# Performance work log

Measured on AMD Instinct MI355X. Metric: run time of the kernel, lower is better.

The kernel has to match this reference:

```python
import jax, jax.numpy as jnp
import numpy as np

B, N, K, D, H, L = 2, 2048, 256, 768, 150, 11
REL_PROP = 2
NB = 10  # distance buckets


def _lin(key, din, dout):
    return jax.random.normal(key, (din, dout), dtype=jnp.float32) / np.sqrt(din)


def setup_inputs() -> dict:
    key = jax.random.key(0)
    ks = jax.random.split(key, 16)
    rng = np.random.default_rng(0)
    prune_idx = jnp.asarray(np.stack([np.sort(rng.permutation(N)[:K]) for _ in range(B)]), dtype=jnp.int32)
    span_begin = jnp.sort(jax.random.randint(ks[2], (B, K), 0, N - 16), axis=-1).astype(jnp.int32)
    span_end = (span_begin + jax.random.randint(ks[3], (B, K), 1, 16)).astype(jnp.int32)
    return {
        "all_span_vecs": jax.random.normal(ks[0], (B, N, D), dtype=jnp.float32),
        "update": jax.random.normal(ks[1], (B, K, D), dtype=jnp.float32),
        "square_mask": jnp.ones((B, K, K), dtype=jnp.float32),
        "span_lengths": jnp.full((B,), float(K), dtype=jnp.float32),
        "span_begin": span_begin,
        "span_end": span_end,
        "prune_indices": prune_idx,
        "w_left": _lin(ks[4], D, H), "b_left": jnp.zeros((H,), jnp.float32),
        "w_right": _lin(ks[5], D, H), "b_right": jnp.zeros((H,), jnp.float32),
        "dist_emb": jax.random.normal(ks[6], (NB, H), dtype=jnp.float32) * 0.02,
        "w_h": _lin(ks[7], H, H), "b_h": jnp.zeros((H,), jnp.float32),
        "w_out": _lin(ks[8], H, L), "b_out": jnp.zeros((L,), jnp.float32),
        "a_w": _lin(ks[9], L, D),
        "gate_w": _lin(ks[10], 2 * D, D), "gate_b": jnp.zeros((D,), jnp.float32),
        "pr_w": _lin(ks[11], D, 1), "pr_b": jnp.zeros((1,), jnp.float32),
    }


def _pair_scores(u, bins, w_left, b_left, w_right, b_right, dist_emb, w_h, b_h, w_out, b_out):
    # OptFFpairs: left/right span projections + pairwise distance embedding -> FF -> L labels
    left = u @ w_left + b_left          # [B,K,H]
    right = u @ w_right + b_right       # [B,K,H]
    h = jax.nn.relu(left[:, :, None, :] + right[:, None, :, :] + dist_emb[bins])  # [B,K,K,H]
    h = jax.nn.relu(h @ w_h + b_h)
    return h @ w_out + b_out            # [B,K,K,L]


def _add_unary(rel, ss):
    # relation_add_scores: add per-span pruner scores along both pair axes; ss: [B,K,1]
    return rel + ss[:, :, None, :] + ss[:, None, :, :]


def reference(all_span_vecs, update, square_mask, span_lengths, span_begin, span_end,
              prune_indices, w_left, b_left, w_right, b_right, dist_emb, w_h, b_h,
              w_out, b_out, a_w, gate_w, gate_b, pr_w, pr_b):
    bins = jnp.clip(jnp.abs(span_begin[:, None, :] - span_begin[:, :, None]), 0, NB - 1)  # [B,K,K]
    rel = _pair_scores(update, bins, w_left, b_left, w_right, b_right, dist_emb, w_h, b_h, w_out, b_out)
    rel = _add_unary(rel, update @ pr_w + pr_b)
    for _ in range(REL_PROP):
        probs = jax.nn.relu(rel) * square_mask[..., None]     # [B,K,K,L]
        msg = probs @ a_w                                     # A(probs): [B,K,K,D]
        # ctxt[b,j,d] = sum_i msg[b,i,j,d] * update[b,i,d] / span_lengths[b]
        ctxt = (msg * update[:, :, None, :]).sum(-3) / span_lengths[:, None, None]
        g = jax.nn.sigmoid(jnp.concatenate([update, ctxt], axis=-1) @ gate_w + gate_b)
        update = g * update + (1.0 - g) * ctxt                # MyGate
        rel = _pair_scores(update, bins, w_left, b_left, w_right, b_right, dist_emb, w_h, b_h, w_out, b_out)
        rel = _add_unary(rel, update @ pr_w + pr_b)           # pruner.scorer(update)
    # overwrite_spans: scatter updated filtered spans back into the full span tensor
    valid = jnp.arange(K)[None, :] < span_lengths[:, None]    # [B,K]
    bidx = jnp.arange(B)[:, None]
    orig = all_span_vecs[bidx, prune_indices]                 # [B,K,D]
    vals = jnp.where(valid[..., None], update, orig)
    update_all = all_span_vecs.at[bidx, prune_indices].set(vals)
    return update_all, update, rel
```

## Files before the change

### kernel.cpp

```cpp
#include <hip/hip_runtime.h>
#include <hip/hip_bf16.h>
#include <math.h>

#define BB 2
#define NN 2048
#define KK 256
#define DD 768
#define HH 150
#define LL 11
#define NBINS 10

#define KP 160
#define WP 40
#define GWP 72
#define BPAD 264

typedef __attribute__((ext_vector_type(8))) short short8;
typedef __attribute__((ext_vector_type(4))) short s16x4;
typedef __attribute__((ext_vector_type(4))) float f32x4;

__device__ inline unsigned bf2u(float lo, float hi) {
  union { __hip_bfloat162 b; unsigned u; } cv;
  cv.b = __float22bfloat162_rn(make_float2(lo, hi));
  return cv.u;
}
__device__ inline short bf1(float x) {
  union { __hip_bfloat16 b; short s; } cv;
  cv.b = __float2bfloat16(x);
  return cv.s;
}

__global__ void k_prep(const float* __restrict__ w_h, const float* __restrict__ w_out,
                       short* __restrict__ wt, short* __restrict__ wo) {
  int idx = blockIdx.x * 256 + threadIdx.x;
  if (idx < KP * KP) {
    int n = idx / KP, k = idx - n * KP;
    float v = (n < HH && k < HH) ? w_h[k * HH + n] : 0.f;
    wt[idx] = bf1(v);
  }
  int idx2 = idx - KP * KP;
  if (idx2 >= 0 && idx2 < 16 * KP) {
    int n = idx2 / KP, k = idx2 - n * KP;
    float v = (n < LL && k < HH) ? w_out[k * LL + n] : 0.f;
    wo[idx2] = bf1(v);
  }
}

__global__ void k_cvt(const float* __restrict__ src, short* __restrict__ dst, int n) {
  int idx = blockIdx.x * 256 + threadIdx.x;
  if (idx < n) dst[idx] = bf1(src[idx]);
}

__global__ __launch_bounds__(256) void k_tr_gw(const float* __restrict__ gate_w,
                                               short* __restrict__ gwt) {
  __shared__ float tile[32][33];
  int kt = blockIdx.x % 48, nt = blockIdx.x / 48;
  int m0 = kt * 32, n0 = nt * 32;
  int tx = threadIdx.x & 31, ty = threadIdx.x >> 5;
  #pragma unroll
  for (int r = 0; r < 4; ++r)
    tile[ty + r * 8][tx] = gate_w[(size_t)(m0 + ty + r * 8) * DD + n0 + tx];
  __syncthreads();
  #pragma unroll
  for (int r = 0; r < 4; ++r)
    gwt[(size_t)(n0 + ty + r * 8) * (2 * DD) + m0 + tx] = bf1(tile[tx][ty + r * 8]);
}

__global__ __launch_bounds__(256) void k_tr_wlr(const float* __restrict__ w_left,
                                                const float* __restrict__ w_right,
                                                short* __restrict__ wlrt) {
  __shared__ float tile[32][33];
  int kt = blockIdx.x % 24, nt = blockIdx.x / 24;
  int k0 = kt * 32, n0 = nt * 32;
  const float* src = (n0 >= KP) ? w_right : w_left;
  int col0 = n0 - (n0 >= KP ? KP : 0);
  int tx = threadIdx.x & 31, ty = threadIdx.x >> 5;
  #pragma unroll
  for (int r = 0; r < 4; ++r) {
    int col = col0 + tx;
    tile[ty + r * 8][tx] = (col < HH) ? src[(size_t)(k0 + ty + r * 8) * HH + col] : 0.f;
  }
  __syncthreads();
  #pragma unroll
  for (int r = 0; r < 4; ++r)
    wlrt[(size_t)(n0 + ty + r * 8) * DD + k0 + tx] = bf1(tile[tx][ty + r * 8]);
}

__global__ __launch_bounds__(256) void k_tr_upd(const float* __restrict__ upd,
                                                short* __restrict__ updT) {
  __shared__ float tile[32][33];
  int bidx = blockIdx.x;
  int b = bidx / 192;
  int r = bidx - b * 192;
  int it = r & 7, dt = r >> 3;
  int i0 = it * 32, d0 = dt * 32;
  int tx = threadIdx.x & 31, ty = threadIdx.x >> 5;
  #pragma unroll
  for (int rr = 0; rr < 4; ++rr)
    tile[ty + rr * 8][tx] = upd[(size_t)(b * KK + i0 + ty + rr * 8) * DD + d0 + tx];
  __syncthreads();
  #pragma unroll
  for (int rr = 0; rr < 4; ++rr)
    updT[(size_t)(b * DD + d0 + ty + rr * 8) * KK + i0 + tx] = bf1(tile[tx][ty + rr * 8]);
}

__global__ __launch_bounds__(256) void k_ptr(const float* __restrict__ rel,
                                             const float* __restrict__ mask,
                                             short* __restrict__ probsT) {
  __shared__ float tile[32][353];
  __shared__ float maskS[32][32];
  int bidx = blockIdx.x;
  int b = bidx >> 6;
  int r = bidx & 63;
  int it = r >> 3, jt = r & 7;
  int i0 = it * 32, j0 = jt * 32;
  int t = threadIdx.x;
  for (int idx = t; idx < 32 * 352; idx += 256) {
    int ii = idx / 352, c = idx - ii * 352;
    tile[ii][c] = rel[(((size_t)(b * KK + i0 + ii)) * KK + j0) * LL + c];
  }
  for (int idx = t; idx < 1024; idx += 256) {
    int ii = idx >> 5, jj = idx & 31;
    maskS[ii][jj] = mask[((size_t)(b * KK + i0 + ii)) * KK + j0 + jj];
  }
  __syncthreads();
  for (int idx = t; idx < LL * 512; idx += 256) {
    int l = idx / 512;
    int rem = idx - l * 512;
    int jj = rem >> 4, ii = (rem & 15) * 2;
    float v0 = fmaxf(tile[ii][jj * LL + l], 0.f) * maskS[ii][jj];
    float v1 = fmaxf(tile[ii + 1][jj * LL + l], 0.f) * maskS[ii + 1][jj];
    *(unsigned*)(probsT + (((size_t)(b * LL + l)) * KK + j0 + jj) * KK + i0 + ii) =
        bf2u(v0, v1);
  }
}

__global__ __launch_bounds__(256) void k_ss(const float* __restrict__ upd,
                                            const float* __restrict__ pr_w,
                                            const float* __restrict__ pr_b,
                                            float* __restrict__ ss) {
  int row = blockIdx.x * 4 + (threadIdx.x >> 6);
  int l = threadIdx.x & 63;
  float s = 0.f;
  for (int d = l; d < DD; d += 64) s = fmaf(upd[(size_t)row * DD + d], pr_w[d], s);
  #pragma unroll
  for (int off = 32; off > 0; off >>= 1) s += __shfl_down(s, off);
  if (l == 0) ss[row] = s + pr_b[0];
}

__global__ __launch_bounds__(256) void k_proj_mfma(
    const short* __restrict__ updbf, const short* __restrict__ wlrt,
    const float* __restrict__ b_left, const float* __restrict__ b_right,
    float* __restrict__ left, float* __restrict__ right)
{
  int rbk = blockIdx.x >> 1, half = blockIdx.x & 1;
  int row0 = rbk * 64;
  const short* wsrc = wlrt + (size_t)half * KP * DD;
  __shared__ short As[64][WP];
  __shared__ short Bs[KP][WP];
  int t = threadIdx.x, l = t & 63, w = t >> 6, lr = l & 15, lg = l >> 4;
  int ar = t >> 2, ac = t & 3;
  int i1 = t + 256, i2 = t + 512;
  f32x4 acc[10];
  #pragma unroll
  for (int nt = 0; nt < 10; ++nt) acc[nt] = (f32x4){0.f, 0.f, 0.f, 0.f};

  short8 pa, pb0, pb1, pb2 = {};
  pa  = *(const short8*)(updbf + (size_t)(row0 + ar) * DD + ac * 8);
  pb0 = *(const short8*)(wsrc + (size_t)(t >> 2) * DD + (t & 3) * 8);
  pb1 = *(const short8*)(wsrc + (size_t)(i1 >> 2) * DD + (i1 & 3) * 8);
  if (i2 < 640) pb2 = *(const short8*)(wsrc + (size_t)(i2 >> 2) * DD + (i2 & 3) * 8);

  for (int ks = 0; ks < 24; ++ks) {
    __syncthreads();
    *(short8*)&As[ar][ac * 8] = pa;
    *(short8*)&Bs[t >> 2][(t & 3) * 8] = pb0;
    *(short8*)&Bs[i1 >> 2][(i1 & 3) * 8] = pb1;
    if (i2 < 640) *(short8*)&Bs[i2 >> 2][(i2 & 3) * 8] = pb2;
    __syncthreads();
    if (ks + 1 < 24) {
      int k0 = (ks + 1) * 32;
      pa  = *(const short8*)(updbf + (size_t)(row0 + ar) * DD + k0 + ac * 8);
      pb0 = *(const short8*)(wsrc + (size_t)(t >> 2) * DD + k0 + (t & 3) * 8);
      pb1 = *(const short8*)(wsrc + (size_t)(i1 >> 2) * DD + k0 + (i1 & 3) * 8);
      if (i2 < 640) pb2 = *(const short8*)(wsrc + (size_t)(i2 >> 2) * DD + k0 + (i2 & 3) * 8);
    }
    short8 a = *(short8*)&As[w * 16 + lr][lg * 8];
    #pragma unroll
    for (int nt = 0; nt < 10; ++nt) {
      short8 b = *(short8*)&Bs[nt * 16 + lr][lg * 8];
      acc[nt] = __builtin_amdgcn_mfma_f32_16x16x32_bf16(a, b, acc[nt], 0, 0, 0);
    }
  }
  const float* bias = half ? b_right : b_left;
  float* dst = half ? right : left;
  int rowb = row0 + w * 16 + lg * 4;
  #pragma unroll
  for (int nt = 0; nt < 10; ++nt) {
    int col = nt * 16 + lr;
    if (col < HH) {
      float bv = bias[col];
      #pragma unroll
      for (int q = 0; q < 4; ++q)
        dst[(size_t)(rowb + q) * HH + col] = acc[nt][q] + bv;
    }
  }
}

__global__ __launch_bounds__(256, 4) void k_pair_mfma(
    const float* __restrict__ left, const float* __restrict__ right,
    const float* __restrict__ ss, const int* __restrict__ span_begin,
    const float* __restrict__ demb,
    const short* __restrict__ wt, const short* __restrict__ wo,
    const float* __restrict__ b_h, const float* __restrict__ b_out,
    float* __restrict__ rel)
{
  int bid = blockIdx.x;
  int b  = bid >> 10;
  int r2 = bid & 1023;
  int i  = r2 >> 2;
  int j0 = (r2 & 3) * 64;

  __shared__ short wtbuf[2][32 * KP];
  __shared__ float ld_s[NBINS][KP];
  __shared__ float bh_s[KP];
  __shared__ float ssj_s[64];
  __shared__ int   bins[64];

  int t = threadIdx.x;
  int l = t & 63, w = t >> 6;
  int lr = l & 15, lg = l >> 4;

  int jr = w * 16 + lr;
  const float* rrow = right + (size_t)(b * KK + j0 + jr) * HH;
  float2 rv[20];
  #pragma unroll
  for (int ks = 0; ks < 5; ++ks) {
    #pragma unroll
    for (int e = 0; e < 4; ++e) {
      int k = ks * 32 + lg * 8 + e * 2;
      rv[ks * 4 + e] = (k < HH - 1) ? *(const float2*)(rrow + k) : make_float2(0.f, 0.f);
    }
  }

  int sbi = span_begin[b * KK + i];
  if (t < 64) {
    int d = span_begin[b * KK + j0 + t] - sbi; d = d < 0 ? -d : d;
    bins[t] = d > NBINS - 1 ? NBINS - 1 : d;
    ssj_s[t] = ss[b * KK + j0 + t];
  }
  for (int idx = t; idx < KP; idx += 256) bh_s[idx] = (idx < HH) ? b_h[idx] : 0.f;
  {
    const float* lrow = left + (size_t)(b * KK + i) * HH;
    for (int idx = t; idx < NBINS * KP; idx += 256) {
      int bn = idx / KP, k = idx - bn * KP;
      ld_s[bn][k] = (k < HH) ? (lrow[k] + demb[bn * HH + k]) : 0.f;
    }
  }
  short8 wo_f[5];
  #pragma unroll
  for (int ks = 0; ks < 5; ++ks)
    wo_f[ks] = *(const short8*)(wo + lr * KP + ks * 32 + lg * 8);

  short8 pw[3];
  #pragma unroll
  for (int c = 0; c < 3; ++c) {
    int idx = t + c * 256;
    if (idx < 640) pw[c] = *(const short8*)(wt + idx * 8);
  }
  #pragma unroll
  for (int c = 0; c < 3; ++c) {
    int idx = t + c * 256;
    if (idx < 640) *(short8*)&wtbuf[0][idx * 8] = pw[c];
  }
  #pragma unroll
  for (int c = 0; c < 3; ++c) {
    int idx = t + c * 256;
    if (idx < 640) pw[c] = *(const short8*)(wt + 5120 + idx * 8);
  }
  __syncthreads();

  int binr = bins[jr];
  const float* ldr = &ld_s[binr][0];
  short8 afr[5];
  #pragma unroll
  for (int ks = 0; ks < 5; ++ks) {
    unsigned pk[4];
    #pragma unroll
    for (int e = 0; e < 4; ++e) {
      int k = ks * 32 + lg * 8 + e * 2;
      float2 lv = *(const float2*)(ldr + k);
      float2 r2v = rv[ks * 4 + e];
      float v0 = fmaxf(lv.x + r2v.x, 0.f);
      float v1 = fmaxf(lv.y + r2v.y, 0.f);
      pk[e] = bf2u(v0, v1);
    }
    int4 tmp; tmp.x = (int)pk[0]; tmp.y = (int)pk[1]; tmp.z = (int)pk[2]; tmp.w = (int)pk[3];
    afr[ks] = *(short8*)&tmp;
  }

  f32x4 acc[10];
  #pragma unroll
  for (int m = 0; m < 10; ++m) acc[m] = (f32x4){0.f, 0.f, 0.f, 0.f};

  #pragma unroll
  for (int s = 0; s < 5; ++s) {
    if (s > 0) __syncthreads();
    if (s + 1 < 5) {
      #pragma unroll
      for (int c = 0; c < 3; ++c) {
        int idx = t + c * 256;
        if (idx < 640) *(short8*)&wtbuf[(s + 1) & 1][idx * 8] = pw[c];
      }
      if (s + 2 < 5) {
        #pragma unroll
        for (int c = 0; c < 3; ++c) {
          int idx = t + c * 256;
          if (idx < 640) pw[c] = *(const short8*)(wt + (s + 2) * 5120 + idx * 8);
        }
      }
    }
    const short* bufp = &wtbuf[s & 1][0];
    #pragma unroll
    for (int ks = 0; ks < 5; ++ks) {
      short8 a = afr[ks];
      #pragma unroll
      for (int ntp = 0; ntp < 2; ++ntp) {
        short8 bf = *(const short8*)(bufp + (ntp * 16 + lr) * KP + ks * 32 + lg * 8);
        acc[s * 2 + ntp] = __builtin_amdgcn_mfma_f32_16x16x32_bf16(a, bf, acc[s * 2 + ntp], 0, 0, 0);
      }
    }
  }
  __syncthreads();

  short* h1 = &wtbuf[0][0];
  #pragma unroll
  for (int m = 0; m < 10; ++m) {
    int col = (m >> 1) * 32 + (m & 1) * 16 + lr;
    float bh = bh_s[col];
    #pragma unroll
    for (int q = 0; q < 4; ++q) {
      int row = w * 16 + lg * 4 + q;
      h1[row * KP + col] = bf1(fmaxf(acc[m][q] + bh, 0.f));
    }
  }
  __syncthreads();

  f32x4 acc2 = (f32x4){0.f, 0.f, 0.f, 0.f};
  #pragma unroll
  for (int ks = 0; ks < 5; ++ks) {
    short8 a = *(const short8*)(h1 + (w * 16 + lr) * KP + ks * 32 + lg * 8);
    acc2 = __builtin_amdgcn_mfma_f32_16x16x32_bf16(a, wo_f[ks], acc2, 0, 0, 0);
  }

  float ssi = ss[b * KK + i];
  float* out_s = (float*)&ld_s[0][0];
  if (lr < LL) {
    float bo = b_out[lr];
    #pragma unroll
    for (int q = 0; q < 4; ++q) {
      int row = w * 16 + lg * 4 + q;
      out_s[row * 12 + lr] = acc2[q] + bo + ssi + ssj_s[row];
    }
  }
  __syncthreads();
  size_t base = ((size_t)(b * KK + i) * KK + j0) * LL;
  for (int idx = t; idx < 64 * LL; idx += 256) {
    int j = idx / LL, ll2 = idx - j * LL;
    rel[base + idx] = out_s[j * 12 + ll2];
  }
}

__global__ __launch_bounds__(256) void k_ctxt_mfma(
    const short* __restrict__ probsT, const short* __restrict__ updT,
    const float* __restrict__ a_w, const float* __restrict__ span_len,
    float* __restrict__ ctxt, short* __restrict__ ctxbf)
{
  int bidx = blockIdx.x;
  int b = bidx / 96;
  int r = bidx - b * 96;
  int jt = r / 12, dt = r - jt * 12;
  int j0 = jt * 32, d0 = dt * 64;

  __shared__ short Bs[64][BPAD];
  __shared__ short As[32][BPAD];

  int t = threadIdx.x, l = t & 63, w = t >> 6, lr = l & 15, lg = l >> 4;
  int wr = w >> 1, wc = w & 1;

  for (int s = 0; s < 8; ++s) {
    int idx = t + s * 256;
    int row = idx >> 5, c = idx & 31;
    *(short8*)&Bs[row][c * 8] =
        *(const short8*)(updT + ((size_t)(b * DD + d0 + row)) * KK + c * 8);
  }

  short8 pa[4];
  #pragma unroll
  for (int s = 0; s < 4; ++s) {
    int idx = t + s * 256;
    int row = idx >> 5, c = idx & 31;
    pa[s] = *(const short8*)(probsT + (((size_t)(b * LL + 0)) * KK + j0 + row) * KK + c * 8);
  }

  f32x4 accF[2];
  accF[0] = (f32x4){0.f, 0.f, 0.f, 0.f};
  accF[1] = (f32x4){0.f, 0.f, 0.f, 0.f};

  for (int ll = 0; ll < LL; ++ll) {
    __syncthreads();
    #pragma unroll
    for (int s = 0; s < 4; ++s) {
      int idx = t + s * 256;
      int row = idx >> 5, c = idx & 31;
      *(short8*)&As[row][c * 8] = pa[s];
    }
    if (ll + 1 < LL) {
      #pragma unroll
      for (int s = 0; s < 4; ++s) {
        int idx = t + s * 256;
        int row = idx >> 5, c = idx & 31;
        pa[s] = *(const short8*)(probsT + (((size_t)(b * LL + ll + 1)) * KK + j0 + row) * KK + c * 8);
      }
    }
    float awl[2];
    #pragma unroll
    for (int nt = 0; nt < 2; ++nt) awl[nt] = a_w[ll * DD + d0 + wc * 32 + nt * 16 + lr];
    __syncthreads();

    f32x4 accL[2];
    accL[0] = (f32x4){0.f, 0.f, 0.f, 0.f};
    accL[1] = (f32x4){0.f, 0.f, 0.f, 0.f};
    #pragma unroll
    for (int ks = 0; ks < 8; ++ks) {
      short8 a = *(short8*)&As[wr * 16 + lr][ks * 32 + lg * 8];
      #pragma unroll
      for (int nt = 0; nt < 2; ++nt) {
        short8 bf = *(short8*)&Bs[wc * 32 + nt * 16 + lr][ks * 32 + lg * 8];
        accL[nt] = __builtin_amdgcn_mfma_f32_16x16x32_bf16(a, bf, accL[nt], 0, 0, 0);
      }
    }
    #pragma unroll
    for (int nt = 0; nt < 2; ++nt)
      #pragma unroll
      for (int q = 0; q < 4; ++q)
        accF[nt][q] = fmaf(awl[nt], accL[nt][q], accF[nt][q]);
  }

  float inv = 1.f / span_len[b];
  int rowb = j0 + wr * 16 + lg * 4;
  #pragma unroll
  for (int nt = 0; nt < 2; ++nt) {
    int col = d0 + wc * 32 + nt * 16 + lr;
    #pragma unroll
    for (int q = 0; q < 4; ++q) {
      size_t off = (size_t)(b * KK + rowb + q) * DD + col;
      float v = accF[nt][q] * inv;
      ctxt[off] = v;
      ctxbf[off] = bf1(v);
    }
  }
}

__global__ __launch_bounds__(256) void k_gate_mfma(
    const short* __restrict__ updbf, const short* __restrict__ ctxbf,
    const short* __restrict__ gwt, const float* __restrict__ gate_b,
    const float* __restrict__ ctxt, float* __restrict__ upd,
    short* __restrict__ nxtbf, short* __restrict__ updT)
{
  int rb = blockIdx.x / 12, cb = blockIdx.x - rb * 12;
  int row0 = rb * 32, col0 = cb * 64;
  __shared__ short As[32][GWP];
  __shared__ short Bs[64][GWP];
  int t = threadIdx.x, l = t & 63, w = t >> 6, lr = l & 15, lg = l >> 4;
  int wr = w >> 1, wc = w & 1;

  int ar = t >> 3, ac = t & 7;
  int b1 = t + 256;

  f32x4 acc[2];
  acc[0] = (f32x4){0.f, 0.f, 0.f, 0.f};
  acc[1] = (f32x4){0.f, 0.f, 0.f, 0.f};

  short8 pa = *(const short8*)(updbf + (size_t)(row0 + ar) * DD + ac * 8);
  short8 pb0 = *(const short8*)(gwt + (size_t)(col0 + (t >> 3)) * (2 * DD) + (t & 7) * 8);
  short8 pb1 = *(const short8*)(gwt + (size_t)(col0 + (b1 >> 3)) * (2 * DD) + (b1 & 7) * 8);

  for (int ks = 0; ks < 24; ++ks) {
    __syncthreads();
    *(short8*)&As[ar][ac * 8] = pa;
    *(short8*)&Bs[t >> 3][(t & 7) * 8] = pb0;
    *(short8*)&Bs[b1 >> 3][(b1 & 7) * 8] = pb1;
    if (ks + 1 < 24) {
      int k0 = (ks + 1) * 64;
      int ka = k0 + ac * 8;
      const short* asrc = (ka < DD) ? (updbf + (size_t)(row0 + ar) * DD + ka)
                                    : (ctxbf + (size_t)(row0 + ar) * DD + ka - DD);
      pa  = *(const short8*)asrc;
      pb0 = *(const short8*)(gwt + (size_t)(col0 + (t >> 3)) * (2 * DD) + k0 + (t & 7) * 8);
      pb1 = *(const short8*)(gwt + (size_t)(col0 + (b1 >> 3)) * (2 * DD) + k0 + (b1 & 7) * 8);
    }
    __syncthreads();
    #pragma unroll
    for (int ksub = 0; ksub < 2; ++ksub) {
      short8 a = *(short8*)&As[wr * 16 + lr][ksub * 32 + lg * 8];
      #pragma unroll
      for (int nt = 0; nt < 2; ++nt) {
        short8 bf = *(short8*)&Bs[wc * 32 + nt * 16 + lr][ksub * 32 + lg * 8];
        acc[nt] = __builtin_amdgcn_mfma_f32_16x16x32_bf16(a, bf, acc[nt], 0, 0, 0);
      }
    }
  }
  int rowb = row0 + wr * 16 + lg * 4;
  int bb = rowb >> 8, ii = rowb & 255;
  #pragma unroll
  for (int nt = 0; nt < 2; ++nt) {
    int col = col0 + wc * 32 + nt * 16 + lr;
    float gb = gate_b[col];
    s16x4 tw;
    #pragma unroll
    for (int q = 0; q < 4; ++q) {
      size_t off = (size_t)(rowb + q) * DD + col;
      float x = acc[nt][q] + gb;
      float g = 1.f / (1.f + expf(-x));
      float o = g * upd[off] + (1.f - g) * ctxt[off];
      upd[off] = o;
      short bv = bf1(o);
      nxtbf[off] = bv;
      tw[q] = bv;
    }
    *(s16x4*)(updT + ((size_t)(bb * DD + col)) * KK + ii) = tw;
  }
}

__global__ void k_scatter(const float* __restrict__ upd,
                          const int* __restrict__ prune_idx,
                          const float* __restrict__ span_len,
                          float* __restrict__ out_all)
{
  int b = blockIdx.x / KK;
  int k = blockIdx.x - b * KK;
  if ((float)k < span_len[b]) {
    int dst = prune_idx[b * KK + k];
    const float4* src = (const float4*)(upd + ((size_t)(b * KK + k)) * DD);
    float4* d = (float4*)(out_all + ((size_t)b * NN + dst) * DD);
    for (int idx = threadIdx.x; idx < DD / 4; idx += blockDim.x) d[idx] = src[idx];
  }
}

extern "C" void kernel_launch(void* const* d_in, const int* in_sizes, int n_in,
                              void* d_out, int out_size, void* d_ws, size_t ws_size,
                              hipStream_t stream)
{
  (void)in_sizes; (void)n_in; (void)out_size; (void)ws_size;
  const float* all_span = (const float*)d_in[0];
  const float* upd_in   = (const float*)d_in[1];
  const float* mask     = (const float*)d_in[2];
  const float* span_len = (const float*)d_in[3];
  const int*   span_beg = (const int*)d_in[4];
  const int*   prune    = (const int*)d_in[6];
  const float* w_left   = (const float*)d_in[7];
  const float* b_left   = (const float*)d_in[8];
  const float* w_right  = (const float*)d_in[9];
  const float* b_right  = (const float*)d_in[10];
  const float* dist_emb = (const float*)d_in[11];
  const float* w_h      = (const float*)d_in[12];
  const float* b_h      = (const float*)d_in[13];
  const float* w_out    = (const float*)d_in[14];
  const float* b_out    = (const float*)d_in[15];
  const float* a_w      = (const float*)d_in[16];
  const float* gate_w   = (const float*)d_in[17];
  const float* gate_b   = (const float*)d_in[18];
  const float* pr_w     = (const float*)d_in[19];
  const float* pr_b     = (const float*)d_in[20];

  float* out_all = (float*)d_out;
  float* out_upd = out_all + (size_t)BB * NN * DD;
  float* out_rel = out_upd + (size_t)BB * KK * DD;

  float* ws     = (float*)d_ws;
  float* left   = ws;
  float* right  = left + (size_t)BB * KK * HH;
  float* ssv    = right + (size_t)BB * KK * HH + 64;
  float* ctxt   = ssv + (size_t)BB * KK;
  short* wt_bf  = (short*)(ctxt + (size_t)BB * KK * DD);
  short* wo_bf  = wt_bf + KP * KP;
  short* updbf0 = wo_bf + 16 * KP;
  short* updbf1 = updbf0 + (size_t)BB * KK * DD;
  short* ctxbf  = updbf1 + (size_t)BB * KK * DD;
  short* gwt    = ctxbf + (size_t)BB * KK * DD;
  short* wlrt   = gwt + (size_t)DD * 2 * DD;
  short* probsT = wlrt + (size_t)2 * KP * DD;
  short* updT   = probsT + (size_t)BB * LL * KK * KK;

  const int nupd = BB * KK * DD;

  hipMemcpyAsync(out_all, all_span, sizeof(float) * (size_t)BB * NN * DD,
                 hipMemcpyDeviceToDevice, stream);
  hipMemcpyAsync(out_upd, upd_in, sizeof(float) * (size_t)BB * KK * DD,
                 hipMemcpyDeviceToDevice, stream);
  k_prep<<<(KP * KP + 16 * KP + 255) / 256, 256, 0, stream>>>(w_h, w_out, wt_bf, wo_bf);
  k_cvt<<<(nupd + 255) / 256, 256, 0, stream>>>(upd_in, updbf0, nupd);
  k_tr_gw<<<48 * 24, 256, 0, stream>>>(gate_w, gwt);
  k_tr_wlr<<<24 * 10, 256, 0, stream>>>(w_left, w_right, wlrt);
  k_tr_upd<<<BB * 8 * 24, 256, 0, stream>>>(upd_in, updT);

  k_proj_mfma<<<16, 256, 0, stream>>>(updbf0, wlrt, b_left, b_right, left, right);
  k_ss<<<BB * KK / 4, 256, 0, stream>>>(out_upd, pr_w, pr_b, ssv);
  k_pair_mfma<<<BB * KK * 4, 256, 0, stream>>>(left, right, ssv, span_beg, dist_emb,
                                               wt_bf, wo_bf, b_h, b_out, out_rel);

  for (int p = 0; p < 2; ++p) {
    short* cur_bf = (p == 0) ? updbf0 : updbf1;
    short* nxt_bf = (p == 0) ? updbf1 : updbf0;
    k_ptr<<<BB * 8 * 8, 256, 0, stream>>>(out_rel, mask, probsT);
    k_ctxt_mfma<<<BB * 8 * 12, 256, 0, stream>>>(probsT, updT, a_w, span_len, ctxt, ctxbf);
    k_gate_mfma<<<16 * 12, 256, 0, stream>>>(cur_bf, ctxbf, gwt, gate_b, ctxt,
                                             out_upd, nxt_bf, updT);
    k_proj_mfma<<<16, 256, 0, stream>>>(nxt_bf, wlrt, b_left, b_right, left, right);
    k_ss<<<BB * KK / 4, 256, 0, stream>>>(out_upd, pr_w, pr_b, ssv);
    k_pair_mfma<<<BB * KK * 4, 256, 0, stream>>>(left, right, ssv, span_beg, dist_emb,
                                                 wt_bf, wo_bf, b_h, b_out, out_rel);
  }
  k_scatter<<<BB * KK, 192, 0, stream>>>(out_upd, prune, span_len, out_all);
}
```

Before: 231.7 us.

## Fuse prep kernels, merge proj with ss, emit probsT from pair kernel

Merges the five preprocessing kernels into one multi-role launch, and folds the unary score reduction into the projection kernel as extra blocks. The pair-score kernel gains a templated epilogue that writes the masked, relu'd, transposed bf16 probabilities directly, removing the separate transpose kernel and its re-read of rel. The right-row operand loads also move from an upfront register array into the inner loop to cut register pressure. The price is strided 2-byte scattered stores for probsT from the pair kernel, and blocks of different roles running inside single launches.

```diff
diff --git a/kernel.cpp b/kernel.cpp
--- a/kernel.cpp
+++ b/kernel.cpp
@@ -30,135 +30,122 @@
   return cv.s;
 }
 
-__global__ void k_prep(const float* __restrict__ w_h, const float* __restrict__ w_out,
-                       short* __restrict__ wt, short* __restrict__ wo) {
-  int idx = blockIdx.x * 256 + threadIdx.x;
-  if (idx < KP * KP) {
-    int n = idx / KP, k = idx - n * KP;
-    float v = (n < HH && k < HH) ? w_h[k * HH + n] : 0.f;
-    wt[idx] = bf1(v);
-  }
-  int idx2 = idx - KP * KP;
-  if (idx2 >= 0 && idx2 < 16 * KP) {
-    int n = idx2 / KP, k = idx2 - n * KP;
-    float v = (n < LL && k < HH) ? w_out[k * LL + n] : 0.f;
-    wo[idx2] = bf1(v);
-  }
-}
-
-__global__ void k_cvt(const float* __restrict__ src, short* __restrict__ dst, int n) {
-  int idx = blockIdx.x * 256 + threadIdx.x;
-  if (idx < n) dst[idx] = bf1(src[idx]);
-}
-
-__global__ __launch_bounds__(256) void k_tr_gw(const float* __restrict__ gate_w,
-                                               short* __restrict__ gwt) {
+#define PRE_PREP 110
+#define PRE_CVT  1536
+#define PRE_TRGW 1152
+#define PRE_TRWLR 240
+#define PRE_TRUPD 384
+#define PRE_NB (PRE_PREP + PRE_CVT + PRE_TRGW + PRE_TRWLR + PRE_TRUPD)
+
+__global__ __launch_bounds__(256) void k_pre(
+    const float* __restrict__ w_h, const float* __restrict__ w_out,
+    short* __restrict__ wt, short* __restrict__ wo,
+    const float* __restrict__ upd_in, short* __restrict__ updbf,
+    const float* __restrict__ gate_w, short* __restrict__ gwt,
+    const float* __restrict__ w_left, const float* __restrict__ w_right,
+    short* __restrict__ wlrt, short* __restrict__ updT)
+{
   __shared__ float tile[32][33];
-  int kt = blockIdx.x % 48, nt = blockIdx.x / 48;
-  int m0 = kt * 32, n0 = nt * 32;
-  int tx = threadIdx.x & 31, ty = threadIdx.x >> 5;
-  #pragma unroll
-  for (int r = 0; r < 4; ++r)
-    tile[ty + r * 8][tx] = gate_w[(size_t)(m0 + ty + r * 8) * DD + n0 + tx];
-  __syncthreads();
-  #pragma unroll
-  for (int r = 0; r < 4; ++r)
-    gwt[(size_t)(n0 + ty + r * 8) * (2 * DD) + m0 + tx] = bf1(tile[tx][ty + r * 8]);
-}
-
-__global__ __launch_bounds__(256) void k_tr_wlr(const float* __restrict__ w_left,
-                                                const float* __restrict__ w_right,
-                                                short* __restrict__ wlrt) {
-  __shared__ float tile[32][33];
-  int kt = blockIdx.x % 24, nt = blockIdx.x / 24;
-  int k0 = kt * 32, n0 = nt * 32;
-  const float* src = (n0 >= KP) ? w_right : w_left;
-  int col0 = n0 - (n0 >= KP ? KP : 0);
-  int tx = threadIdx.x & 31, ty = threadIdx.x >> 5;
-  #pragma unroll
-  for (int r = 0; r < 4; ++r) {
-    int col = col0 + tx;
-    tile[ty + r * 8][tx] = (col < HH) ? src[(size_t)(k0 + ty + r * 8) * HH + col] : 0.f;
-  }
-  __syncthreads();
-  #pragma unroll
-  for (int r = 0; r < 4; ++r)
-    wlrt[(size_t)(n0 + ty + r * 8) * DD + k0 + tx] = bf1(tile[tx][ty + r * 8]);
-}
-
-__global__ __launch_bounds__(256) void k_tr_upd(const float* __restrict__ upd,
-                                                short* __restrict__ updT) {
-  __shared__ float tile[32][33];
-  int bidx = blockIdx.x;
-  int b = bidx / 192;
-  int r = bidx - b * 192;
-  int it = r & 7, dt = r >> 3;
-  int i0 = it * 32, d0 = dt * 32;
-  int tx = threadIdx.x & 31, ty = threadIdx.x >> 5;
-  #pragma unroll
-  for (int rr = 0; rr < 4; ++rr)
-    tile[ty + rr * 8][tx] = upd[(size_t)(b * KK + i0 + ty + rr * 8) * DD + d0 + tx];
-  __syncthreads();
-  #pragma unroll
-  for (int rr = 0; rr < 4; ++rr)
-    updT[(size_t)(b * DD + d0 + ty + rr * 8) * KK + i0 + tx] = bf1(tile[tx][ty + rr * 8]);
-}
-
-__global__ __launch_bounds__(256) void k_ptr(const float* __restrict__ rel,
-                                             const float* __restrict__ mask,
-                                             short* __restrict__ probsT) {
-  __shared__ float tile[32][353];
-  __shared__ float maskS[32][32];
-  int bidx = blockIdx.x;
-  int b = bidx >> 6;
-  int r = bidx & 63;
-  int it = r >> 3, jt = r & 7;
-  int i0 = it * 32, j0 = jt * 32;
+  int bid = blockIdx.x;
   int t = threadIdx.x;
-  for (int idx = t; idx < 32 * 352; idx += 256) {
-    int ii = idx / 352, c = idx - ii * 352;
-    tile[ii][c] = rel[(((size_t)(b * KK + i0 + ii)) * KK + j0) * LL + c];
-  }
-  for (int idx = t; idx < 1024; idx += 256) {
-    int ii = idx >> 5, jj = idx & 31;
-    maskS[ii][jj] = mask[((size_t)(b * KK + i0 + ii)) * KK + j0 + jj];
-  }
-  __syncthreads();
-  for (int idx = t; idx < LL * 512; idx += 256) {
-    int l = idx / 512;
-    int rem = idx - l * 512;
-    int jj = rem >> 4, ii = (rem & 15) * 2;
-    float v0 = fmaxf(tile[ii][jj * LL + l], 0.f) * maskS[ii][jj];
-    float v1 = fmaxf(tile[ii + 1][jj * LL + l], 0.f) * maskS[ii + 1][jj];
-    *(unsigned*)(probsT + (((size_t)(b * LL + l)) * KK + j0 + jj) * KK + i0 + ii) =
-        bf2u(v0, v1);
-  }
-}
-
-__global__ __launch_bounds__(256) void k_ss(const float* __restrict__ upd,
-                                            const float* __restrict__ pr_w,
-                                            const float* __restrict__ pr_b,
-                                            float* __restrict__ ss) {
-  int row = blockIdx.x * 4 + (threadIdx.x >> 6);
-  int l = threadIdx.x & 63;
-  float s = 0.f;
-  for (int d = l; d < DD; d += 64) s = fmaf(upd[(size_t)row * DD + d], pr_w[d], s);
-  #pragma unroll
-  for (int off = 32; off > 0; off >>= 1) s += __shfl_down(s, off);
-  if (l == 0) ss[row] = s + pr_b[0];
-}
-
-__global__ __launch_bounds__(256) void k_proj_mfma(
+
+  if (bid < PRE_PREP) {
+    int idx = bid * 256 + t;
+    if (idx < KP * KP) {
+      int n = idx / KP, k = idx - n * KP;
+      float v = (n < HH && k < HH) ? w_h[k * HH + n] : 0.f;
+      wt[idx] = bf1(v);
+    }
+    int idx2 = idx - KP * KP;
+    if (idx2 >= 0 && idx2 < 16 * KP) {
+      int n = idx2 / KP, k = idx2 - n * KP;
+      float v = (n < LL && k < HH) ? w_out[k * LL + n] : 0.f;
+      wo[idx2] = bf1(v);
+    }
+    return;
+  }
+  bid -= PRE_PREP;
+  if (bid < PRE_CVT) {
+    int idx = bid * 256 + t;
+    if (idx < BB * KK * DD) updbf[idx] = bf1(upd_in[idx]);
+    return;
+  }
+  bid -= PRE_CVT;
+  if (bid < PRE_TRGW) {
+    int kt = bid % 48, nt = bid / 48;
+    int m0 = kt * 32, n0 = nt * 32;
+    int tx = t & 31, ty = t >> 5;
+    #pragma unroll
+    for (int r = 0; r < 4; ++r)
+      tile[ty + r * 8][tx] = gate_w[(size_t)(m0 + ty + r * 8) * DD + n0 + tx];
+    __syncthreads();
+    #pragma unroll
+    for (int r = 0; r < 4; ++r)
+      gwt[(size_t)(n0 + ty + r * 8) * (2 * DD) + m0 + tx] = bf1(tile[tx][ty + r * 8]);
+    return;
+  }
+  bid -= PRE_TRGW;
+  if (bid < PRE_TRWLR) {
+    int kt = bid % 24, nt = bid / 24;
+    int k0 = kt * 32, n0 = nt * 32;
+    const float* src = (n0 >= KP) ? w_right : w_left;
+    int col0 = n0 - (n0 >= KP ? KP : 0);
+    int tx = t & 31, ty = t >> 5;
+    #pragma unroll
+    for (int r = 0; r < 4; ++r) {
+      int col = col0 + tx;
+      tile[ty + r * 8][tx] = (col < HH) ? src[(size_t)(k0 + ty + r * 8) * HH + col] : 0.f;
+    }
+    __syncthreads();
+    #pragma unroll
+    for (int r = 0; r < 4; ++r)
+      wlrt[(size_t)(n0 + ty + r * 8) * DD + k0 + tx] = bf1(tile[tx][ty + r * 8]);
+    return;
+  }
+  bid -= PRE_TRWLR;
+  {
+    int b = bid / 192;
+    int r = bid - b * 192;
+    int it = r & 7, dt = r >> 3;
+    int i0 = it * 32, d0 = dt * 32;
+    int tx = t & 31, ty = t >> 5;
+    #pragma unroll
+    for (int rr = 0; rr < 4; ++rr)
+      tile[ty + rr * 8][tx] = upd_in[(size_t)(b * KK + i0 + ty + rr * 8) * DD + d0 + tx];
+    __syncthreads();
+    #pragma unroll
+    for (int rr = 0; rr < 4; ++rr)
+      updT[(size_t)(b * DD + d0 + ty + rr * 8) * KK + i0 + tx] = bf1(tile[tx][ty + rr * 8]);
+  }
+}
+
+__global__ __launch_bounds__(256) void k_projss(
     const short* __restrict__ updbf, const short* __restrict__ wlrt,
     const float* __restrict__ b_left, const float* __restrict__ b_right,
-    float* __restrict__ left, float* __restrict__ right)
+    const float* __restrict__ updf, const float* __restrict__ pr_w,
+    const float* __restrict__ pr_b,
+    float* __restrict__ left, float* __restrict__ right, float* __restrict__ ssv)
 {
-  int rbk = blockIdx.x >> 1, half = blockIdx.x & 1;
+  __shared__ short As[64][WP];
+  __shared__ short Bs[KP][WP];
+  int bidx = blockIdx.x;
+  int t = threadIdx.x;
+
+  if (bidx >= 16) {
+    int row = (bidx - 16) * 4 + (t >> 6);
+    int l = t & 63;
+    float s = 0.f;
+    for (int d = l; d < DD; d += 64) s = fmaf(updf[(size_t)row * DD + d], pr_w[d], s);
+    #pragma unroll
+    for (int off = 32; off > 0; off >>= 1) s += __shfl_down(s, off);
+    if (l == 0) ssv[row] = s + pr_b[0];
+    return;
+  }
+
+  int rbk = bidx >> 1, half = bidx & 1;
   int row0 = rbk * 64;
   const short* wsrc = wlrt + (size_t)half * KP * DD;
-  __shared__ short As[64][WP];
-  __shared__ short Bs[KP][WP];
-  int t = threadIdx.x, l = t & 63, w = t >> 6, lr = l & 15, lg = l >> 4;
+  int l = t & 63, w = t >> 6, lr = l & 15, lg = l >> 4;
   int ar = t >> 2, ac = t & 3;
   int i1 = t + 256, i2 = t + 512;
   f32x4 acc[10];
@@ -207,13 +194,15 @@
   }
 }
 
+template <bool WPT>
 __global__ __launch_bounds__(256, 4) void k_pair_mfma(
     const float* __restrict__ left, const float* __restrict__ right,
     const float* __restrict__ ss, const int* __restrict__ span_begin,
     const float* __restrict__ demb,
     const short* __restrict__ wt, const short* __restrict__ wo,
     const float* __restrict__ b_h, const float* __restrict__ b_out,
-    float* __restrict__ rel)
+    const float* __restrict__ mask,
+    float* __restrict__ rel, short* __restrict__ probsT)
 {
   int bid = blockIdx.x;
   int b  = bid >> 10;
@@ -225,29 +214,19 @@
   __shared__ float ld_s[NBINS][KP];
   __shared__ float bh_s[KP];
   __shared__ float ssj_s[64];
+  __shared__ float m_s[64];
   __shared__ int   bins[64];
 
   int t = threadIdx.x;
   int l = t & 63, w = t >> 6;
   int lr = l & 15, lg = l >> 4;
-
-  int jr = w * 16 + lr;
-  const float* rrow = right + (size_t)(b * KK + j0 + jr) * HH;
-  float2 rv[20];
-  #pragma unroll
-  for (int ks = 0; ks < 5; ++ks) {
-    #pragma unroll
-    for (int e = 0; e < 4; ++e) {
-      int k = ks * 32 + lg * 8 + e * 2;
-      rv[ks * 4 + e] = (k < HH - 1) ? *(const float2*)(rrow + k) : make_float2(0.f, 0.f);
-    }
-  }
 
   int sbi = span_begin[b * KK + i];
   if (t < 64) {
     int d = span_begin[b * KK + j0 + t] - sbi; d = d < 0 ? -d : d;
     bins[t] = d > NBINS - 1 ? NBINS - 1 : d;
     ssj_s[t] = ss[b * KK + j0 + t];
+    if (WPT) m_s[t] = mask[((size_t)(b * KK + i)) * KK + j0 + t];
   }
   for (int idx = t; idx < KP; idx += 256) bh_s[idx] = (idx < HH) ? b_h[idx] : 0.f;
   {
@@ -280,7 +259,9 @@
   }
   __syncthreads();
 
+  int jr = w * 16 + lr;
   int binr = bins[jr];
+  const float* rrow = right + (size_t)(b * KK + j0 + jr) * HH;
   const float* ldr = &ld_s[binr][0];
   short8 afr[5];
   #pragma unroll
@@ -289,8 +270,8 @@
     #pragma unroll
     for (int e = 0; e < 4; ++e) {
       int k = ks * 32 + lg * 8 + e * 2;
+      float2 r2v = (k < HH - 1) ? *(const float2*)(rrow + k) : make_float2(0.f, 0.f);
       float2 lv = *(const float2*)(ldr + k);
-      float2 r2v = rv[ks * 4 + e];
       float v0 = fmaxf(lv.x + r2v.x, 0.f);
       float v1 = fmaxf(lv.y + r2v.y, 0.f);
       pk[e] = bf2u(v0, v1);
@@ -368,6 +349,13 @@
   for (int idx = t; idx < 64 * LL; idx += 256) {
     int j = idx / LL, ll2 = idx - j * LL;
     rel[base + idx] = out_s[j * 12 + ll2];
+  }
+  if (WPT) {
+    for (int idx = t; idx < 64 * LL; idx += 256) {
+      int j = idx / LL, ll2 = idx - j * LL;
+      float v = fmaxf(out_s[j * 12 + ll2], 0.f) * m_s[j];
+      probsT[(((size_t)(b * LL + ll2)) * KK + j0 + j) * KK + i] = bf1(v);
+    }
   }
 }
 
@@ -593,34 +581,36 @@
   short* probsT = wlrt + (size_t)2 * KP * DD;
   short* updT   = probsT + (size_t)BB * LL * KK * KK;
 
-  const int nupd = BB * KK * DD;
-
   hipMemcpyAsync(out_all, all_span, sizeof(float) * (size_t)BB * NN * DD,
                  hipMemcpyDeviceToDevice, stream);
   hipMemcpyAsync(out_upd, upd_in, sizeof(float) * (size_t)BB * KK * DD,
                  hipMemcpyDeviceToDevice, stream);
-  k_prep<<<(KP * KP + 16 * KP + 255) / 256, 256, 0, stream>>>(w_h, w_out, wt_bf, wo_bf);
-  k_cvt<<<(nupd + 255) / 256, 256, 0, stream>>>(upd_in, updbf0, nupd);
-  k_tr_gw<<<48 * 24, 256, 0, stream>>>(gate_w, gwt);
-  k_tr_wlr<<<24 * 10, 256, 0, stream>>>(w_left, w_right, wlrt);
-  k_tr_upd<<<BB * 8 * 24, 256, 0, stream>>>(upd_in, updT);
-
-  k_proj_mfma<<<16, 256, 0, stream>>>(updbf0, wlrt, b_left, b_right, left, right);
-  k_ss<<<BB * KK / 4, 256, 0, stream>>>(out_upd, pr_w, pr_b, ssv);
-  k_pair_mfma<<<BB * KK * 4, 256, 0, stream>>>(left, right, ssv, span_beg, dist_emb,
-                                               wt_bf, wo_bf, b_h, b_out, out_rel);
+  k_pre<<<PRE_NB, 256, 0, stream>>>(w_h, w_out, wt_bf, wo_bf, upd_in, updbf0,
+                                    gate_w, gwt, w_left, w_right, wlrt, updT);
+
+  k_projss<<<144, 256, 0, stream>>>(updbf0, wlrt, b_left, b_right, out_upd,
+                                    pr_w, pr_b, left, right, ssv);
+  k_pair_mfma<true><<<BB * KK * 4, 256, 0, stream>>>(
+      left, right, ssv, span_beg, dist_emb, wt_bf, wo_bf, b_h, b_out, mask,
+      out_rel, probsT);
 
   for (int p = 0; p < 2; ++p) {
     short* cur_bf = (p == 0) ? updbf0 : updbf1;
     short* nxt_bf = (p == 0) ? updbf1 : updbf0;
-    k_ptr<<<BB * 8 * 8, 256, 0, stream>>>(out_rel, mask, probsT);
     k_ctxt_mfma<<<BB * 8 * 12, 256, 0, stream>>>(probsT, updT, a_w, span_len, ctxt, ctxbf);
     k_gate_mfma<<<16 * 12, 256, 0, stream>>>(cur_bf, ctxbf, gwt, gate_b, ctxt,
                                              out_upd, nxt_bf, updT);
-    k_proj_mfma<<<16, 256, 0, stream>>>(nxt_bf, wlrt, b_left, b_right, left, right);
-    k_ss<<<BB * KK / 4, 256, 0, stream>>>(out_upd, pr_w, pr_b, ssv);
-    k_pair_mfma<<<BB * KK * 4, 256, 0, stream>>>(left, right, ssv, span_beg, dist_emb,
-                                                 wt_bf, wo_bf, b_h, b_out, out_rel);
+    k_projss<<<144, 256, 0, stream>>>(nxt_bf, wlrt, b_left, b_right, out_upd,
+                                      pr_w, pr_b, left, right, ssv);
+    if (p == 0) {
+      k_pair_mfma<true><<<BB * KK * 4, 256, 0, stream>>>(
+          left, right, ssv, span_beg, dist_emb, wt_bf, wo_bf, b_h, b_out, mask,
+          out_rel, probsT);
+    } else {
+      k_pair_mfma<false><<<BB * KK * 4, 256, 0, stream>>>(
+          left, right, ssv, span_beg, dist_emb, wt_bf, wo_bf, b_h, b_out, mask,
+          out_rel, probsT);
+    }
   }
   k_scatter<<<BB * KK, 192, 0, stream>>>(out_upd, prune, span_len, out_all);
 }
```

New measurement: 194.8 us. 1.19x faster.
